# Performance work log

Hardware: AMD Instinct MI355X
Metric: run time of the kernel (lower is better)

The kernel has to match this reference:

```python
import jax, jax.numpy as jnp
import numpy as np

N = 50000   # nodes
E = 800000  # edges (avg degree 16)
F_IN = 128
H = 128
L = 4
LN_EPS = 1e-5


def setup_inputs() -> dict:
    key = jax.random.key(0)
    ks = jax.random.split(key, 4)
    x = jax.random.normal(ks[0], (N, F_IN), dtype=jnp.float32)
    edge_index = jax.random.randint(ks[1], (2, E), 0, N)
    conv_w = jax.random.normal(ks[2], (L, F_IN, H), dtype=jnp.float32) * 0.05
    conv_b = jnp.zeros((L, H), dtype=jnp.float32)
    ln_g = jnp.ones((L, H), dtype=jnp.float32)
    ln_b = jnp.zeros((L, H), dtype=jnp.float32)
    head_w = jax.random.normal(ks[3], (H, 1), dtype=jnp.float32) * 0.05
    head_b = jnp.zeros((1,), dtype=jnp.float32)
    return {"x": x, "edge_index": edge_index, "conv_w": conv_w, "conv_b": conv_b,
            "ln_g": ln_g, "ln_b": ln_b, "head_w": head_w, "head_b": head_b}


def _layer_norm(h, g, b):
    mu = jnp.mean(h, axis=-1, keepdims=True)
    var = jnp.mean(jnp.square(h - mu), axis=-1, keepdims=True)
    return (h - mu) * jax.lax.rsqrt(var + LN_EPS) * g + b


def _gcn_conv(h, W, b, src, dst, inv_sqrt_deg, inv_deg):
    # PyG GCNConv: self-loops + symmetric normalization D^-1/2 (A+I) D^-1/2, then bias.
    hw = h @ W  # (N, H)
    norm = inv_sqrt_deg[src] * inv_sqrt_deg[dst]  # (E,)
    msg = hw[src] * norm[:, None]  # gather + edgewise scale
    agg = jax.ops.segment_sum(msg, dst, num_segments=N)  # scatter-add
    agg = agg + hw * inv_deg[:, None]  # self-loop term (norm = 1/deg)
    return agg + b


def reference(x, edge_index, conv_w, conv_b, ln_g, ln_b, head_w, head_b):
    src, dst = edge_index[0], edge_index[1]
    # degree on target nodes, including self-loop
    deg = jax.ops.segment_sum(jnp.ones((E,), x.dtype), dst, num_segments=N) + 1.0
    inv_sqrt_deg = jax.lax.rsqrt(deg)
    inv_deg = 1.0 / deg
    h = x
    for i in range(L):
        h = _gcn_conv(h, conv_w[i], conv_b[i], src, dst, inv_sqrt_deg, inv_deg)
        h = _layer_norm(h, ln_g[i], ln_b[i])
        if i != L - 1:
            h = jax.nn.gelu(h, approximate=False)
            # dropout is identity in eval mode
    scores = (h @ head_w + head_b).squeeze(-1)  # (N,)
    return scores, h
```

## Files before the change

### kernel.cpp

```cpp
#include <hip/hip_runtime.h>
#include <math.h>

#define N_NODES 50000
#define N_EDGES 800000
#define HDIM 128
#define NLAYERS 4
#define LN_EPS 1e-5f

typedef __attribute__((ext_vector_type(8))) short short8;
typedef __attribute__((ext_vector_type(4))) float floatx4;

__device__ __forceinline__ ushort f2bf(float x) {
    unsigned b = __float_as_uint(x);
    unsigned r = b + 0x7fffu + ((b >> 16) & 1u);
    return (ushort)(r >> 16);
}
__device__ __forceinline__ float2 bf2f2(unsigned u) {
    return make_float2(__uint_as_float(u << 16), __uint_as_float(u & 0xffff0000u));
}


__global__ void deg_count_kernel(const int* __restrict__ dst, int* __restrict__ degcnt) {
    int e = blockIdx.x * blockDim.x + threadIdx.x;
    if (e < N_EDGES) atomicAdd(&degcnt[dst[e]], 1);
}

__global__ __launch_bounds__(256) void alloc_kernel(
    const int* __restrict__ degcnt, int* __restrict__ counter,
    int* __restrict__ start, int* __restrict__ cursor,
    float* __restrict__ isd, float* __restrict__ ind) {
    int i = blockIdx.x * 256 + threadIdx.x;
    int lane = threadIdx.x & 63;
    int deg = (i < N_NODES) ? degcnt[i] : 0;
    int v = deg;
#pragma unroll
    for (int off = 1; off < 64; off <<= 1) {
        int t = __shfl_up(v, off);
        if (lane >= off) v += t;
    }
    int total = __shfl(v, 63);
    int base = 0;
    if (lane == 63) base = atomicAdd(counter, total);
    base = __shfl(base, 63);
    if (i < N_NODES) {
        int st = base + v - deg;
        start[i] = st;
        cursor[i] = st;
        float d = (float)deg + 1.0f;
        isd[i] = rsqrtf(d);
        ind[i] = 1.0f / d;
    }
}

__global__ void fill_kernel(const int* __restrict__ src, const int* __restrict__ dst,
                            int* __restrict__ cursor, ushort* __restrict__ csr16) {
    int e = blockIdx.x * blockDim.x + threadIdx.x;
    if (e < N_EDGES) {
        int s = src[e], d = dst[e];
        int p = atomicAdd(&cursor[d], 1);
        csr16[p] = (ushort)s;
    }
}

__global__ __launch_bounds__(256) void bprep_kernel(const float* __restrict__ W,
                                                    ushort* __restrict__ bfrag) {
    int idx = blockIdx.x * 256 + threadIdx.x;
    if (idx >= NLAYERS * 4 * 8 * 64) return;
    int lane = idx & 63;
    int t = (idx >> 6) & 7;
    int s = (idx >> 9) & 3;
    int l = idx >> 11;
    int n = t * 16 + (lane & 15);
    int kb = s * 32 + (lane >> 4) * 8;
    const float* Wl = W + (size_t)l * HDIM * HDIM;
    union { uint4 q; ushort u[8]; } o;
#pragma unroll
    for (int j = 0; j < 8; ++j) o.u[j] = f2bf(Wl[(size_t)(kb + j) * HDIM + n]);
    *(uint4*)&bfrag[(size_t)idx * 8] = o.q;
}

template <bool A_FP32>
__global__ __launch_bounds__(256) void gemm_mfma_kernel(const void* __restrict__ Av,
                                                        const ushort* __restrict__ bfrag,
                                                        ushort* __restrict__ out) {
    int wave = threadIdx.x >> 6, lane = threadIdx.x & 63;
    int quad = lane >> 4, mrow = lane & 15;
    int rowBase = blockIdx.x * 64 + wave * 16;
    int arow = rowBase + mrow;
    bool aok = arow < N_NODES;

    floatx4 acc[8];
#pragma unroll
    for (int t = 0; t < 8; ++t) acc[t] = (floatx4)0.f;

#pragma unroll
    for (int s = 0; s < 4; ++s) {
        union { short8 v; ushort u[8]; } af;
        if (A_FP32) {
            const float* A = (const float*)Av;
            if (aok) {
                const float* p = &A[(size_t)arow * HDIM + s * 32 + quad * 8];
#pragma unroll
                for (int j = 0; j < 8; ++j) af.u[j] = f2bf(p[j]);
            } else {
#pragma unroll
                for (int j = 0; j < 8; ++j) af.u[j] = 0;
            }
        } else {
            const ushort* A = (const ushort*)Av;
            if (aok) {
                af.v = *(const short8*)&A[(size_t)arow * HDIM + s * 32 + quad * 8];
            } else {
#pragma unroll
                for (int j = 0; j < 8; ++j) af.u[j] = 0;
            }
        }
#pragma unroll
        for (int t = 0; t < 8; ++t) {
            short8 bf = *(const short8*)&bfrag[(size_t)(((s * 8 + t) * 64) + lane) * 8];
            acc[t] = __builtin_amdgcn_mfma_f32_16x16x32_bf16(af.v, bf, acc[t], 0, 0, 0);
        }
    }
#pragma unroll
    for (int t = 0; t < 8; ++t) {
#pragma unroll
        for (int r = 0; r < 4; ++r) {
            int row = rowBase + quad * 4 + r;
            if (row < N_NODES) out[(size_t)row * HDIM + t * 16 + mrow] = f2bf(acc[t][r]);
        }
    }
}

__global__ __launch_bounds__(256) void agg_ln_kernel(
    const unsigned* __restrict__ hwu, const int* __restrict__ start,
    const int* __restrict__ degcnt, const ushort* __restrict__ csr16,
    const float* __restrict__ isd, const float* __restrict__ ind,
    const float* __restrict__ conv_b, const float* __restrict__ ln_g,
    const float* __restrict__ ln_b, unsigned* __restrict__ hout_bf,
    float* __restrict__ hout_f32, const float* __restrict__ head_w,
    const float* __restrict__ head_b, float* __restrict__ scores,
    int final_layer) {
    int wave = threadIdx.x >> 6;
    int lane = threadIdx.x & 63;
    int n = blockIdx.x * 4 + wave;
    if (n >= N_NODES) return;
    int c = lane * 2;

    float2 hv = bf2f2(hwu[(size_t)n * 64 + lane]);
    float isd_n = isd[n];
    float ind_n = ind[n];
    int rs = start[n];
    int deg = degcnt[n];

    float ex = 0.f, ey = 0.f;
    for (int b0 = 0; b0 < deg; b0 += 64) {
        int m = deg - b0;
        if (m > 64) m = 64;
        int sj = 0;
        float wj = 0.f;
        if (lane < m) {
            sj = (int)csr16[rs + b0 + lane];
            wj = isd[sj];
        }
        for (int j = 0; j < m; j += 8) {
            int s0 = __shfl(sj, j + 0), s1 = __shfl(sj, j + 1);
            int s2 = __shfl(sj, j + 2), s3 = __shfl(sj, j + 3);
            int s4 = __shfl(sj, j + 4), s5 = __shfl(sj, j + 5);
            int s6 = __shfl(sj, j + 6), s7 = __shfl(sj, j + 7);
            float w0 = __shfl(wj, j + 0), w1 = __shfl(wj, j + 1);
            float w2 = __shfl(wj, j + 2), w3 = __shfl(wj, j + 3);
            float w4 = __shfl(wj, j + 4), w5 = __shfl(wj, j + 5);
            float w6 = __shfl(wj, j + 6), w7 = __shfl(wj, j + 7);
            unsigned u0 = hwu[(size_t)s0 * 64 + lane];
            unsigned u1 = hwu[(size_t)s1 * 64 + lane];
            unsigned u2 = hwu[(size_t)s2 * 64 + lane];
            unsigned u3 = hwu[(size_t)s3 * 64 + lane];
            unsigned u4 = hwu[(size_t)s4 * 64 + lane];
            unsigned u5 = hwu[(size_t)s5 * 64 + lane];
            unsigned u6 = hwu[(size_t)s6 * 64 + lane];
            unsigned u7 = hwu[(size_t)s7 * 64 + lane];
            float2 v0 = bf2f2(u0), v1 = bf2f2(u1), v2 = bf2f2(u2), v3 = bf2f2(u3);
            float2 v4 = bf2f2(u4), v5 = bf2f2(u5), v6 = bf2f2(u6), v7 = bf2f2(u7);
            ex = fmaf(v0.x, w0, ex); ey = fmaf(v0.y, w0, ey);
            ex = fmaf(v1.x, w1, ex); ey = fmaf(v1.y, w1, ey);
            ex = fmaf(v2.x, w2, ex); ey = fmaf(v2.y, w2, ey);
            ex = fmaf(v3.x, w3, ex); ey = fmaf(v3.y, w3, ey);
            ex = fmaf(v4.x, w4, ex); ey = fmaf(v4.y, w4, ey);
            ex = fmaf(v5.x, w5, ex); ey = fmaf(v5.y, w5, ey);
            ex = fmaf(v6.x, w6, ex); ey = fmaf(v6.y, w6, ey);
            ex = fmaf(v7.x, w7, ex); ey = fmaf(v7.y, w7, ey);
        }
    }
    float2 cb = *(const float2*)&conv_b[c];
    float ax = fmaf(ex, isd_n, fmaf(hv.x, ind_n, cb.x));
    float ay = fmaf(ey, isd_n, fmaf(hv.y, ind_n, cb.y));

    float sum = ax + ay;
#pragma unroll
    for (int o = 32; o; o >>= 1) sum += __shfl_xor(sum, o);
    float mu = sum * (1.0f / HDIM);
    float dx = ax - mu, dy = ay - mu;
    float vs = dx * dx + dy * dy;
#pragma unroll
    for (int o = 32; o; o >>= 1) vs += __shfl_xor(vs, o);
    float rstd = rsqrtf(vs * (1.0f / HDIM) + LN_EPS);
    float2 g = *(const float2*)&ln_g[c];
    float2 b = *(const float2*)&ln_b[c];
    float yx = fmaf(dx * rstd, g.x, b.x);
    float yy = fmaf(dy * rstd, g.y, b.y);

    if (!final_layer) {
        yx = 0.5f * yx * (1.0f + erff(yx * 0.70710678118654752f));
        yy = 0.5f * yy * (1.0f + erff(yy * 0.70710678118654752f));
        hout_bf[(size_t)n * 64 + lane] = (unsigned)f2bf(yx) | ((unsigned)f2bf(yy) << 16);
    } else {
        *(float2*)&hout_f32[(size_t)n * HDIM + c] = make_float2(yx, yy);
        float2 hwv = *(const float2*)&head_w[c];
        float p = yx * hwv.x + yy * hwv.y;
#pragma unroll
        for (int o = 32; o; o >>= 1) p += __shfl_xor(p, o);
        if (lane == 0) scores[n] = p + head_b[0];
    }
}


extern "C" void kernel_launch(void* const* d_in, const int* in_sizes, int n_in,
                              void* d_out, int out_size, void* d_ws, size_t ws_size,
                              hipStream_t stream) {
    const float* x      = (const float*)d_in[0];
    const int*   eidx   = (const int*)d_in[1];
    const float* conv_w = (const float*)d_in[2];
    const float* conv_b = (const float*)d_in[3];
    const float* ln_g   = (const float*)d_in[4];
    const float* ln_b   = (const float*)d_in[5];
    const float* head_w = (const float*)d_in[6];
    const float* head_b = (const float*)d_in[7];
    float* out = (float*)d_out;

    const int* src = eidx;
    const int* dst = eidx + N_EDGES;

    char* ws = (char*)d_ws;
    size_t o = 0;
    auto alloc = [&](size_t elems) {
        void* p = ws + o * 4;
        o += (elems + 15) & ~(size_t)15;
        return p;
    };
    int*      degcnt   = (int*)alloc(N_NODES);
    int*      counter  = (int*)alloc(16);
    float*    isd      = (float*)alloc(N_NODES);
    float*    ind      = (float*)alloc(N_NODES);
    int*      start    = (int*)alloc(N_NODES);
    int*      cursor   = (int*)alloc(N_NODES);
    ushort*   csr16    = (ushort*)alloc(N_EDGES / 2);
    ushort*   bfrag    = (ushort*)alloc(NLAYERS * 4 * 8 * 64 * 8 / 2);
    unsigned* hw       = (unsigned*)alloc((size_t)N_NODES * 64);
    unsigned* hbuf     = (unsigned*)alloc((size_t)N_NODES * 64);

    hipMemsetAsync(degcnt, 0, (N_NODES + 16) * sizeof(int), stream);
    deg_count_kernel<<<(N_EDGES + 255) / 256, 256, 0, stream>>>(dst, degcnt);
    int nblk = (N_NODES + 255) / 256;
    alloc_kernel<<<nblk, 256, 0, stream>>>(degcnt, counter, start, cursor, isd, ind);
    fill_kernel<<<(N_EDGES + 255) / 256, 256, 0, stream>>>(src, dst, cursor, csr16);
    bprep_kernel<<<(NLAYERS * 4 * 8 * 64 + 255) / 256, 256, 0, stream>>>(conv_w, bfrag);

    const void* hin = (const void*)x;
    for (int l = 0; l < NLAYERS; ++l) {
        const ushort* bl = bfrag + (size_t)l * 4 * 8 * 64 * 8;
        if (l == 0)
            gemm_mfma_kernel<true><<<(N_NODES + 63) / 64, 256, 0, stream>>>(hin, bl, (ushort*)hw);
        else
            gemm_mfma_kernel<false><<<(N_NODES + 63) / 64, 256, 0, stream>>>(hin, bl, (ushort*)hw);
        int fin = (l == NLAYERS - 1) ? 1 : 0;
        agg_ln_kernel<<<(N_NODES + 3) / 4, 256, 0, stream>>>(
            hw, start, degcnt, csr16, isd, ind,
            conv_b + (size_t)l * HDIM, ln_g + (size_t)l * HDIM, ln_b + (size_t)l * HDIM,
            hbuf, out + N_NODES, head_w, head_b, out, fin);
        hin = (const void*)hbuf;
    }
}
```

Baseline: 370.0 us.

## Process four nodes per wave with 16-lane groups and 16-byte gathers

The aggregation+LayerNorm kernel now assigns 16 lanes per node, so four nodes share a wave, and each lane gathers 8 bf16 features with a 128-bit load instead of 2 with a 32-bit load. Neighbor loops run up to the maximum degree across the wave's four nodes. Reductions shrink to 16-lane butterflies. This cuts per-edge load instruction count and raises bytes in flight per instruction. The cost is divergence when the four nodes have unequal degrees, and the grid now assumes N divisible by 16 with no bounds check.

```diff
diff --git a/kernel.cpp b/kernel.cpp
--- a/kernel.cpp
+++ b/kernel.cpp
@@ -132,95 +132,124 @@
 }
 
 __global__ __launch_bounds__(256) void agg_ln_kernel(
-    const unsigned* __restrict__ hwu, const int* __restrict__ start,
+    const uint4* __restrict__ hw4, const int* __restrict__ start,
     const int* __restrict__ degcnt, const ushort* __restrict__ csr16,
     const float* __restrict__ isd, const float* __restrict__ ind,
     const float* __restrict__ conv_b, const float* __restrict__ ln_g,
-    const float* __restrict__ ln_b, unsigned* __restrict__ hout_bf,
+    const float* __restrict__ ln_b, uint4* __restrict__ hout_bf,
     float* __restrict__ hout_f32, const float* __restrict__ head_w,
     const float* __restrict__ head_b, float* __restrict__ scores,
     int final_layer) {
     int wave = threadIdx.x >> 6;
     int lane = threadIdx.x & 63;
-    int n = blockIdx.x * 4 + wave;
-    if (n >= N_NODES) return;
-    int c = lane * 2;
-
-    float2 hv = bf2f2(hwu[(size_t)n * 64 + lane]);
-    float isd_n = isd[n];
-    float ind_n = ind[n];
-    int rs = start[n];
-    int deg = degcnt[n];
-
-    float ex = 0.f, ey = 0.f;
-    for (int b0 = 0; b0 < deg; b0 += 64) {
-        int m = deg - b0;
-        if (m > 64) m = 64;
+    int lin = lane & 15;
+    int gbase = lane & 48;
+    int n = blockIdx.x * 16 + wave * 4 + (lane >> 4);
+    int c = lin * 8;
+
+    float ind_n = ind[n], isd_n = isd[n];
+    int rs = start[n], deg = degcnt[n];
+    uint4 hv = hw4[(size_t)n * 16 + lin];
+
+    float e0 = 0.f, e1 = 0.f, e2 = 0.f, e3 = 0.f, e4 = 0.f, e5 = 0.f, e6 = 0.f, e7 = 0.f;
+
+    int dmax = deg;
+#pragma unroll
+    for (int o = 1; o < 64; o <<= 1) dmax = max(dmax, __shfl_xor(dmax, o));
+
+#define ACC8(U, W)                                                         \
+    {                                                                      \
+        float2 q0 = bf2f2((U).x), q1 = bf2f2((U).y);                       \
+        float2 q2 = bf2f2((U).z), q3 = bf2f2((U).w);                       \
+        e0 = fmaf(q0.x, (W), e0); e1 = fmaf(q0.y, (W), e1);                \
+        e2 = fmaf(q1.x, (W), e2); e3 = fmaf(q1.y, (W), e3);                \
+        e4 = fmaf(q2.x, (W), e4); e5 = fmaf(q2.y, (W), e5);                \
+        e6 = fmaf(q3.x, (W), e6); e7 = fmaf(q3.y, (W), e7);                \
+    }
+
+    for (int b0 = 0; b0 < dmax; b0 += 16) {
+        int rem = deg - b0;
         int sj = 0;
         float wj = 0.f;
-        if (lane < m) {
-            sj = (int)csr16[rs + b0 + lane];
+        if (lin < rem) {
+            sj = (int)csr16[rs + b0 + lin];
             wj = isd[sj];
         }
-        for (int j = 0; j < m; j += 8) {
-            int s0 = __shfl(sj, j + 0), s1 = __shfl(sj, j + 1);
-            int s2 = __shfl(sj, j + 2), s3 = __shfl(sj, j + 3);
-            int s4 = __shfl(sj, j + 4), s5 = __shfl(sj, j + 5);
-            int s6 = __shfl(sj, j + 6), s7 = __shfl(sj, j + 7);
-            float w0 = __shfl(wj, j + 0), w1 = __shfl(wj, j + 1);
-            float w2 = __shfl(wj, j + 2), w3 = __shfl(wj, j + 3);
-            float w4 = __shfl(wj, j + 4), w5 = __shfl(wj, j + 5);
-            float w6 = __shfl(wj, j + 6), w7 = __shfl(wj, j + 7);
-            unsigned u0 = hwu[(size_t)s0 * 64 + lane];
-            unsigned u1 = hwu[(size_t)s1 * 64 + lane];
-            unsigned u2 = hwu[(size_t)s2 * 64 + lane];
-            unsigned u3 = hwu[(size_t)s3 * 64 + lane];
-            unsigned u4 = hwu[(size_t)s4 * 64 + lane];
-            unsigned u5 = hwu[(size_t)s5 * 64 + lane];
-            unsigned u6 = hwu[(size_t)s6 * 64 + lane];
-            unsigned u7 = hwu[(size_t)s7 * 64 + lane];
-            float2 v0 = bf2f2(u0), v1 = bf2f2(u1), v2 = bf2f2(u2), v3 = bf2f2(u3);
-            float2 v4 = bf2f2(u4), v5 = bf2f2(u5), v6 = bf2f2(u6), v7 = bf2f2(u7);
-            ex = fmaf(v0.x, w0, ex); ey = fmaf(v0.y, w0, ey);
-            ex = fmaf(v1.x, w1, ex); ey = fmaf(v1.y, w1, ey);
-            ex = fmaf(v2.x, w2, ex); ey = fmaf(v2.y, w2, ey);
-            ex = fmaf(v3.x, w3, ex); ey = fmaf(v3.y, w3, ey);
-            ex = fmaf(v4.x, w4, ex); ey = fmaf(v4.y, w4, ey);
-            ex = fmaf(v5.x, w5, ex); ey = fmaf(v5.y, w5, ey);
-            ex = fmaf(v6.x, w6, ex); ey = fmaf(v6.y, w6, ey);
-            ex = fmaf(v7.x, w7, ex); ey = fmaf(v7.y, w7, ey);
-        }
-    }
-    float2 cb = *(const float2*)&conv_b[c];
-    float ax = fmaf(ex, isd_n, fmaf(hv.x, ind_n, cb.x));
-    float ay = fmaf(ey, isd_n, fmaf(hv.y, ind_n, cb.y));
-
-    float sum = ax + ay;
-#pragma unroll
-    for (int o = 32; o; o >>= 1) sum += __shfl_xor(sum, o);
+#pragma unroll
+        for (int j = 0; j < 16; j += 4) {
+            int s0 = __shfl(sj, gbase + j + 0), s1 = __shfl(sj, gbase + j + 1);
+            int s2 = __shfl(sj, gbase + j + 2), s3 = __shfl(sj, gbase + j + 3);
+            float w0 = __shfl(wj, gbase + j + 0), w1 = __shfl(wj, gbase + j + 1);
+            float w2 = __shfl(wj, gbase + j + 2), w3 = __shfl(wj, gbase + j + 3);
+            uint4 u0 = hw4[(size_t)s0 * 16 + lin];
+            uint4 u1 = hw4[(size_t)s1 * 16 + lin];
+            uint4 u2 = hw4[(size_t)s2 * 16 + lin];
+            uint4 u3 = hw4[(size_t)s3 * 16 + lin];
+            ACC8(u0, w0);
+            ACC8(u1, w1);
+            ACC8(u2, w2);
+            ACC8(u3, w3);
+        }
+    }
+
+    float4 cb0 = *(const float4*)&conv_b[c];
+    float4 cb1 = *(const float4*)&conv_b[c + 4];
+    float2 h0 = bf2f2(hv.x), h1 = bf2f2(hv.y), h2 = bf2f2(hv.z), h3 = bf2f2(hv.w);
+    float a0 = fmaf(e0, isd_n, fmaf(h0.x, ind_n, cb0.x));
+    float a1 = fmaf(e1, isd_n, fmaf(h0.y, ind_n, cb0.y));
+    float a2 = fmaf(e2, isd_n, fmaf(h1.x, ind_n, cb0.z));
+    float a3 = fmaf(e3, isd_n, fmaf(h1.y, ind_n, cb0.w));
+    float a4 = fmaf(e4, isd_n, fmaf(h2.x, ind_n, cb1.x));
+    float a5 = fmaf(e5, isd_n, fmaf(h2.y, ind_n, cb1.y));
+    float a6 = fmaf(e6, isd_n, fmaf(h3.x, ind_n, cb1.z));
+    float a7 = fmaf(e7, isd_n, fmaf(h3.y, ind_n, cb1.w));
+
+    float sum = a0 + a1 + a2 + a3 + a4 + a5 + a6 + a7;
+#pragma unroll
+    for (int o = 1; o < 16; o <<= 1) sum += __shfl_xor(sum, o);
     float mu = sum * (1.0f / HDIM);
-    float dx = ax - mu, dy = ay - mu;
-    float vs = dx * dx + dy * dy;
-#pragma unroll
-    for (int o = 32; o; o >>= 1) vs += __shfl_xor(vs, o);
+    float d0 = a0 - mu, d1 = a1 - mu, d2 = a2 - mu, d3 = a3 - mu;
+    float d4 = a4 - mu, d5 = a5 - mu, d6 = a6 - mu, d7 = a7 - mu;
+    float vs = d0 * d0 + d1 * d1 + d2 * d2 + d3 * d3 + d4 * d4 + d5 * d5 + d6 * d6 + d7 * d7;
+#pragma unroll
+    for (int o = 1; o < 16; o <<= 1) vs += __shfl_xor(vs, o);
     float rstd = rsqrtf(vs * (1.0f / HDIM) + LN_EPS);
-    float2 g = *(const float2*)&ln_g[c];
-    float2 b = *(const float2*)&ln_b[c];
-    float yx = fmaf(dx * rstd, g.x, b.x);
-    float yy = fmaf(dy * rstd, g.y, b.y);
+    float4 g0 = *(const float4*)&ln_g[c];
+    float4 g1 = *(const float4*)&ln_g[c + 4];
+    float4 b0v = *(const float4*)&ln_b[c];
+    float4 b1v = *(const float4*)&ln_b[c + 4];
+    float y0 = fmaf(d0 * rstd, g0.x, b0v.x);
+    float y1 = fmaf(d1 * rstd, g0.y, b0v.y);
+    float y2 = fmaf(d2 * rstd, g0.z, b0v.z);
+    float y3 = fmaf(d3 * rstd, g0.w, b0v.w);
+    float y4 = fmaf(d4 * rstd, g1.x, b1v.x);
+    float y5 = fmaf(d5 * rstd, g1.y, b1v.y);
+    float y6 = fmaf(d6 * rstd, g1.z, b1v.z);
+    float y7 = fmaf(d7 * rstd, g1.w, b1v.w);
 
     if (!final_layer) {
-        yx = 0.5f * yx * (1.0f + erff(yx * 0.70710678118654752f));
-        yy = 0.5f * yy * (1.0f + erff(yy * 0.70710678118654752f));
-        hout_bf[(size_t)n * 64 + lane] = (unsigned)f2bf(yx) | ((unsigned)f2bf(yy) << 16);
+#define GELU(v) ((v) = 0.5f * (v) * (1.0f + erff((v) * 0.70710678118654752f)))
+        GELU(y0); GELU(y1); GELU(y2); GELU(y3);
+        GELU(y4); GELU(y5); GELU(y6); GELU(y7);
+#undef GELU
+        uint4 ov;
+        ov.x = (unsigned)f2bf(y0) | ((unsigned)f2bf(y1) << 16);
+        ov.y = (unsigned)f2bf(y2) | ((unsigned)f2bf(y3) << 16);
+        ov.z = (unsigned)f2bf(y4) | ((unsigned)f2bf(y5) << 16);
+        ov.w = (unsigned)f2bf(y6) | ((unsigned)f2bf(y7) << 16);
+        hout_bf[(size_t)n * 16 + lin] = ov;
     } else {
-        *(float2*)&hout_f32[(size_t)n * HDIM + c] = make_float2(yx, yy);
-        float2 hwv = *(const float2*)&head_w[c];
-        float p = yx * hwv.x + yy * hwv.y;
-#pragma unroll
-        for (int o = 32; o; o >>= 1) p += __shfl_xor(p, o);
-        if (lane == 0) scores[n] = p + head_b[0];
-    }
+        *(float4*)&hout_f32[(size_t)n * HDIM + c] = make_float4(y0, y1, y2, y3);
+        *(float4*)&hout_f32[(size_t)n * HDIM + c + 4] = make_float4(y4, y5, y6, y7);
+        float4 hw0 = *(const float4*)&head_w[c];
+        float4 hw1 = *(const float4*)&head_w[c + 4];
+        float p = y0 * hw0.x + y1 * hw0.y + y2 * hw0.z + y3 * hw0.w +
+                  y4 * hw1.x + y5 * hw1.y + y6 * hw1.z + y7 * hw1.w;
+#pragma unroll
+        for (int o = 1; o < 16; o <<= 1) p += __shfl_xor(p, o);
+        if (lin == 0) scores[n] = p + head_b[0];
+    }
+#undef ACC8
 }
 
 
@@ -273,10 +302,10 @@
         else
             gemm_mfma_kernel<false><<<(N_NODES + 63) / 64, 256, 0, stream>>>(hin, bl, (ushort*)hw);
         int fin = (l == NLAYERS - 1) ? 1 : 0;
-        agg_ln_kernel<<<(N_NODES + 3) / 4, 256, 0, stream>>>(
-            hw, start, degcnt, csr16, isd, ind,
+        agg_ln_kernel<<<N_NODES / 16, 256, 0, stream>>>(
+            (const uint4*)hw, start, degcnt, csr16, isd, ind,
             conv_b + (size_t)l * HDIM, ln_g + (size_t)l * HDIM, ln_b + (size_t)l * HDIM,
-            hbuf, out + N_NODES, head_w, head_b, out, fin);
+            (uint4*)hbuf, out + N_NODES, head_w, head_b, out, fin);
         hin = (const void*)hbuf;
     }
 }
```

Result: slower. 393.6 us (+6.4%).
